# Kernel tuning notes

Hardware: AMD Instinct MI355X
Metric: run time of the kernel (lower is better)

## Reference

```python
import jax, jax.numpy as jnp
import numpy as np

N = 100_000        # nodes
E = 1_600_000      # edges (avg degree 16)
NODE_DIM = 64
HIDDEN = 64
OUT = 32


def _glorot(key, fan_in, fan_out):
    lim = np.sqrt(6.0 / (fan_in + fan_out)).astype(np.float32)
    return jax.random.uniform(key, (fan_in, fan_out), jnp.float32, -lim, lim)


def setup_inputs() -> dict:
    key = jax.random.key(0)
    ks = jax.random.split(key, 5)
    x = jax.random.normal(ks[0], (N, NODE_DIM), jnp.float32)
    edge_index = jax.random.randint(ks[1], (2, E), 0, N, dtype=jnp.int64)
    return {
        "x": x,
        "edge_index": edge_index,
        "W1": _glorot(ks[2], NODE_DIM, HIDDEN),
        "b1": jnp.zeros((HIDDEN,), jnp.float32),
        "Wmu": _glorot(ks[3], HIDDEN, OUT),
        "bmu": jnp.zeros((OUT,), jnp.float32),
        "Wlv": _glorot(ks[4], HIDDEN, OUT),
        "blv": jnp.zeros((OUT,), jnp.float32),
    }


def _gcn_conv(h, W, b, src, dst, norm, n):
    """PyG GCNConv: linear (no bias) -> normalized scatter-add -> + bias.
    src/dst/norm already include self-loops and deg^{-1/2} symmetric norm."""
    h = h @ W                                   # [n, out]
    msg = h[src] * norm[:, None]                # [E+N, out] gather
    out = jax.ops.segment_sum(msg, dst, num_segments=n)  # scatter-add
    return out + b


def reference(x, edge_index, W1, b1, Wmu, bmu, Wlv, blv):
    loops = jnp.arange(N, dtype=edge_index.dtype)
    src = jnp.concatenate([edge_index[0], loops])  # add self-loops
    dst = jnp.concatenate([edge_index[1], loops])
    # symmetric normalization: deg computed on target nodes (all weights 1)
    deg = jax.ops.segment_sum(jnp.ones_like(src, dtype=x.dtype), dst, num_segments=N)
    dinv = jax.lax.rsqrt(deg)                   # deg >= 1 due to self-loops
    norm = dinv[src] * dinv[dst]

    h = jax.nn.relu(_gcn_conv(x, W1, b1, src, dst, norm, N))
    mu = _gcn_conv(h, Wmu, bmu, src, dst, norm, N)
    logvar = _gcn_conv(h, Wlv, blv, src, dst, norm, N)
    return mu, logvar
```

## Files before the change

### kernel.cpp

```cpp
#include <hip/hip_runtime.h>
#include <hip/hip_fp16.h>


#define BKT_SHIFT 9
#define BKT_NODES 512
#define CHUNK 2048

typedef __attribute__((ext_vector_type(8))) _Float16 half8;
typedef __attribute__((ext_vector_type(4))) float float4v;
typedef __attribute__((ext_vector_type(4))) unsigned uint4v;

__device__ __forceinline__ int imin(int a, int b) { return a < b ? a : b; }
__device__ __forceinline__ int imax(int a, int b) { return a > b ? a : b; }
__device__ __forceinline__ unsigned h2u(__half2 v) {
  union { __half2 h; unsigned u; } c; c.h = v; return c.u;
}
__device__ __forceinline__ __half2 u2h(unsigned x) {
  union { unsigned u; __half2 h; } c; c.u = x; return c.h;
}


__global__ __launch_bounds__(1024) void block_sums(const int* __restrict__ in,
                                                   int* __restrict__ bsum, int n) {
  __shared__ int s[1024];
  int t = threadIdx.x;
  int i = blockIdx.x * 1024 + t;
  s[t] = (i < n) ? in[i] : 0;
  __syncthreads();
  for (int off = 512; off > 0; off >>= 1) {
    if (t < off) s[t] += s[t + off];
    __syncthreads();
  }
  if (t == 0) bsum[blockIdx.x] = s[0];
}

__global__ __launch_bounds__(1024) void scan_bsums(int* __restrict__ bsum, int nb) {
  __shared__ int s[1024];
  int t = threadIdx.x;
  int v = (t < nb) ? bsum[t] : 0;
  s[t] = v;
  __syncthreads();
  for (int off = 1; off < 1024; off <<= 1) {
    int u = (t >= off) ? s[t - off] : 0;
    __syncthreads();
    s[t] += u;
    __syncthreads();
  }
  if (t < nb) bsum[t] = s[t] - v;
}

__global__ __launch_bounds__(1024) void scan_apply(int* __restrict__ data,
                                                   const int* __restrict__ bofs, int n) {
  __shared__ int s[1024];
  int t = threadIdx.x;
  int i = blockIdx.x * 1024 + t;
  int c = (i < n) ? data[i] : 0;
  s[t] = c;
  __syncthreads();
  for (int off = 1; off < 1024; off <<= 1) {
    int u = (t >= off) ? s[t - off] : 0;
    __syncthreads();
    s[t] += u;
    __syncthreads();
  }
  if (i < n) data[i] = bofs[blockIdx.x] + s[t] - c;
}


__global__ __launch_bounds__(256) void bucket_count(const int* __restrict__ dst,
                                                    int* __restrict__ cnt,
                                                    int E, int nbk, int nblk) {
  __shared__ int hist[2][256];
  const int t = threadIdx.x;
  const int h = (t >> 7) & 1;
  hist[0][t] = 0;
  hist[1][t] = 0;
  __syncthreads();
  const int base = blockIdx.x * CHUNK;
  const int end = imin(base + CHUNK, E);
  for (int e = base + t * 4; e < end; e += 1024) {
    if (e + 3 < end) {
      const int4 d4 = *(const int4*)(dst + e);
      atomicAdd(&hist[h][d4.x >> BKT_SHIFT], 1);
      atomicAdd(&hist[h][d4.y >> BKT_SHIFT], 1);
      atomicAdd(&hist[h][d4.z >> BKT_SHIFT], 1);
      atomicAdd(&hist[h][d4.w >> BKT_SHIFT], 1);
    } else {
      for (int k = e; k < end; ++k) atomicAdd(&hist[h][dst[k] >> BKT_SHIFT], 1);
    }
  }
  __syncthreads();
  if (t < nbk) cnt[t * nblk + blockIdx.x] = hist[0][t] + hist[1][t];
}

__global__ __launch_bounds__(256) void bucket_scatter(const int* __restrict__ src,
                                                      const int* __restrict__ dst,
                                                      const int* __restrict__ ofs,
                                                      int2* __restrict__ tmp,
                                                      int E, int nbk, int nblk) {
  __shared__ int cur[256];
  const int t = threadIdx.x;
  if (t < nbk) cur[t] = ofs[t * nblk + blockIdx.x];
  __syncthreads();
  const int base = blockIdx.x * CHUNK;
  const int end = imin(base + CHUNK, E);
  for (int e = base + t * 4; e < end; e += 1024) {
    if (e + 3 < end) {
      const int4 s4 = *(const int4*)(src + e);
      const int4 d4 = *(const int4*)(dst + e);
      int p0 = atomicAdd(&cur[d4.x >> BKT_SHIFT], 1);
      tmp[p0] = make_int2(s4.x, d4.x);
      int p1 = atomicAdd(&cur[d4.y >> BKT_SHIFT], 1);
      tmp[p1] = make_int2(s4.y, d4.y);
      int p2 = atomicAdd(&cur[d4.z >> BKT_SHIFT], 1);
      tmp[p2] = make_int2(s4.z, d4.z);
      int p3 = atomicAdd(&cur[d4.w >> BKT_SHIFT], 1);
      tmp[p3] = make_int2(s4.w, d4.w);
    } else {
      for (int k = e; k < end; ++k) {
        int d = dst[k];
        int pos = atomicAdd(&cur[d >> BKT_SHIFT], 1);
        tmp[pos] = make_int2(src[k], d);
      }
    }
  }
}

__global__ __launch_bounds__(512) void bucket_build(const int2* __restrict__ tmp,
                                                    const int* __restrict__ ofs,
                                                    int* __restrict__ row_ptr,
                                                    float* __restrict__ dinv,
                                                    int* __restrict__ pairs,
                                                    int n, int nbk, int nblk, int E) {
  __shared__ int hist[BKT_NODES];
  __shared__ int scn[BKT_NODES];
  const int b = blockIdx.x;
  const int t = threadIdx.x;
  const int node0 = b << BKT_SHIFT;
  hist[t] = 0;
  __syncthreads();
  const int s = ofs[b * nblk];
  const int e = (b + 1 < nbk) ? ofs[(b + 1) * nblk] : E;
  for (int k = s + t; k < e; k += 512) atomicAdd(&hist[tmp[k].y - node0], 1);
  __syncthreads();
  const int v = hist[t];
  scn[t] = v;
  __syncthreads();
  for (int off = 1; off < 512; off <<= 1) {
    int u = (t >= off) ? scn[t - off] : 0;
    __syncthreads();
    scn[t] += u;
    __syncthreads();
  }
  const int excl = s + scn[t] - v;
  const int node = node0 + t;
  if (node < n) {
    row_ptr[node] = excl;
    dinv[node] = rsqrtf(1.0f + (float)v);
  }
  if (b == nbk - 1 && t == 0) row_ptr[n] = E;
  hist[t] = excl;
  __syncthreads();
  for (int k = s + t; k < e; k += 512) {
    int2 p = tmp[k];
    int pos = atomicAdd(&hist[p.y - node0], 1);
    pairs[pos] = p.x;
  }
}

__global__ __launch_bounds__(256) void cast_scale(const float* __restrict__ x,
                                                  const float* __restrict__ dinv,
                                                  __half* __restrict__ xs,
                                                  __half* __restrict__ hs,
                                                  int n4, int nrow) {
  int i = blockIdx.x * blockDim.x + threadIdx.x;
  if (i < n4) {
    float4 v = ((const float4*)x)[i];
    float d = dinv[i >> 4];
    __half2* o = (__half2*)(xs + (size_t)i * 4);
    o[0] = __floats2half2_rn(d * v.x, d * v.y);
    o[1] = __floats2half2_rn(d * v.z, d * v.w);
  } else if (i < n4 + 32) {
    int j = i - n4;
    if (j < 16)
      ((float2*)(xs + (size_t)nrow * 64))[j] = make_float2(0.f, 0.f);
    else
      ((float2*)(hs + (size_t)nrow * 64))[j - 16] = make_float2(0.f, 0.f);
  }
}


#define YSTRIDE 264

__global__ __launch_bounds__(256, 4) void agg_layer1(const __half* __restrict__ xs,
                                                     const int* __restrict__ pairs,
                                                     const int* __restrict__ row_ptr,
                                                     const float* __restrict__ W1,
                                                     const float* __restrict__ b1,
                                                     __half* __restrict__ hs, int n) {
  __shared__ _Float16 ylds_all[4][16 * YSTRIDE];
  __shared__ float dilds_all[4][16];
  const int wv = threadIdx.x >> 6;
  _Float16* ylds = ylds_all[wv];
  float* dilds = dilds_all[wv];
  const int lane = threadIdx.x & 63;
  const int g = lane >> 3, q = lane & 7;
  const int quad = lane >> 4, col = lane & 15;

  half8 bfrag[2][4];
#pragma unroll
  for (int s = 0; s < 2; ++s)
#pragma unroll
    for (int t = 0; t < 4; ++t)
#pragma unroll
      for (int jj = 0; jj < 8; ++jj)
        bfrag[s][t][jj] = (_Float16)W1[(s * 32 + quad * 8 + jj) * 64 + t * 16 + col];
  float bias[4];
#pragma unroll
  for (int t = 0; t < 4; ++t) bias[t] = b1[t * 16 + col];

  const int ntiles = (n + 15) >> 4;
  for (int tile = blockIdx.x * 4 + wv; tile < ntiles; tile += gridDim.x * 4) {
    const int row0 = tile << 4;
#pragma unroll 1
    for (int rg = 0; rg < 4; ++rg) {
      int start[4], end[4], idx[4];
      __half2 acc[4][4];
      int maxdeg = 0;
#pragma unroll
      for (int j = 0; j < 4; ++j) {
        const int i = row0 + rg * 4 + j;
        start[j] = 0; end[j] = 0;
        if (i < n) { start[j] = row_ptr[i]; end[j] = row_ptr[i + 1]; }
        maxdeg = imax(maxdeg, end[j] - start[j]);
#pragma unroll
        for (int k = 0; k < 4; ++k) acc[j][k] = u2h(0u);
        idx[j] = (start[j] + g < end[j]) ? pairs[start[j] + g] : n;
      }
      const int iters = (maxdeg + 7) >> 3;
#pragma unroll 1
      for (int it = 0; it < iters; ++it) {
        int nidx[4];
#pragma unroll
        for (int j = 0; j < 4; ++j) {
          const int ofs2 = start[j] + (it + 1) * 8 + g;
          nidx[j] = (ofs2 < end[j]) ? pairs[ofs2] : n;
        }
#pragma unroll
        for (int j = 0; j < 4; ++j) {
          const float4 rr = *(const float4*)(xs + (size_t)idx[j] * 64 + q * 8);
          const __half2* hp = (const __half2*)&rr;
#pragma unroll
          for (int k = 0; k < 4; ++k) acc[j][k] = __hadd2(acc[j][k], hp[k]);
        }
#pragma unroll
        for (int j = 0; j < 4; ++j) idx[j] = nidx[j];
      }
#pragma unroll
      for (int j = 0; j < 4; ++j) {
        const int i = row0 + rg * 4 + j;
        if (g == 0 && i < n) {
          const float4 sr = *(const float4*)(xs + (size_t)i * 64 + q * 8);
          const __half2* hp = (const __half2*)&sr;
#pragma unroll
          for (int k = 0; k < 4; ++k) acc[j][k] = __hadd2(acc[j][k], hp[k]);
        }
#pragma unroll
        for (int k = 0; k < 4; ++k) {
          unsigned u = __shfl_xor(h2u(acc[j][k]), 32);
          acc[j][k] = __hadd2(acc[j][k], u2h(u));
        }
        const float di = rsqrtf((float)(1 + end[j] - start[j]));
        const __half hdi = __float2half(di);
        const __half2 di2 = __halves2half2(hdi, hdi);
        uint4v st;
        st.x = h2u(__hmul2(di2, acc[j][0]));
        st.y = h2u(__hmul2(di2, acc[j][1]));
        st.z = h2u(__hmul2(di2, acc[j][2]));
        st.w = h2u(__hmul2(di2, acc[j][3]));
        *(uint4v*)(ylds + (rg * 4 + j) * YSTRIDE + (g & 3) * 64 + q * 8) = st;
        if (lane == 0) dilds[rg * 4 + j] = di;
      }
    }
    float4v acc[4];
#pragma unroll
    for (int t = 0; t < 4; ++t) acc[t] = (float4v){bias[t], bias[t], bias[t], bias[t]};
#pragma unroll
    for (int s2 = 0; s2 < 8; ++s2) {
      half8 af = *(half8*)(ylds + col * YSTRIDE + s2 * 32 + quad * 8);
      const int sW = s2 & 1;
#pragma unroll
      for (int t = 0; t < 4; ++t)
        acc[t] = __builtin_amdgcn_mfma_f32_16x16x32_f16(af, bfrag[sW][t], acc[t], 0, 0, 0);
    }
    const float4 dis = *(const float4*)(dilds + quad * 4);
    const float dd[4] = {dis.x, dis.y, dis.z, dis.w};
#pragma unroll
    for (int t = 0; t < 4; ++t)
#pragma unroll
      for (int reg = 0; reg < 4; ++reg) {
        const int row = row0 + quad * 4 + reg;
        if (row < n)
          hs[(size_t)row * 64 + t * 16 + col] =
              __float2half(dd[reg] * fmaxf(acc[t][reg], 0.f));
      }
  }
}

__global__ __launch_bounds__(256, 4) void agg_layer2(const __half* __restrict__ hsin,
                                                     const int* __restrict__ pairs,
                                                     const int* __restrict__ row_ptr,
                                                     const float* __restrict__ Wmu,
                                                     const float* __restrict__ bmu,
                                                     const float* __restrict__ Wlv,
                                                     const float* __restrict__ blv,
                                                     float* __restrict__ out_mu,
                                                     float* __restrict__ out_lv, int n) {
  __shared__ _Float16 ylds_all[4][16 * YSTRIDE];
  const int wv = threadIdx.x >> 6;
  _Float16* ylds = ylds_all[wv];
  const int lane = threadIdx.x & 63;
  const int g = lane >> 3, q = lane & 7;
  const int quad = lane >> 4, col = lane & 15;

  half8 bfrag[2][4];
#pragma unroll
  for (int s = 0; s < 2; ++s)
#pragma unroll
    for (int t = 0; t < 4; ++t) {
      const int j = t * 16 + col;
      const float* W = (j < 32) ? Wmu : Wlv;
      const int jc = j & 31;
#pragma unroll
      for (int jj = 0; jj < 8; ++jj)
        bfrag[s][t][jj] = (_Float16)W[(s * 32 + quad * 8 + jj) * 32 + jc];
    }
  float bias[4];
#pragma unroll
  for (int t = 0; t < 4; ++t) {
    const int j = t * 16 + col;
    bias[t] = (j < 32) ? bmu[j] : blv[j - 32];
  }

  const int ntiles = (n + 15) >> 4;
  for (int tile = blockIdx.x * 4 + wv; tile < ntiles; tile += gridDim.x * 4) {
    const int row0 = tile << 4;
#pragma unroll 1
    for (int rg = 0; rg < 4; ++rg) {
      int start[4], end[4], idx[4];
      __half2 acc[4][4];
      int maxdeg = 0;
#pragma unroll
      for (int j = 0; j < 4; ++j) {
        const int i = row0 + rg * 4 + j;
        start[j] = 0; end[j] = 0;
        if (i < n) { start[j] = row_ptr[i]; end[j] = row_ptr[i + 1]; }
        maxdeg = imax(maxdeg, end[j] - start[j]);
#pragma unroll
        for (int k = 0; k < 4; ++k) acc[j][k] = u2h(0u);
        idx[j] = (start[j] + g < end[j]) ? pairs[start[j] + g] : n;
      }
      const int iters = (maxdeg + 7) >> 3;
#pragma unroll 1
      for (int it = 0; it < iters; ++it) {
        int nidx[4];
#pragma unroll
        for (int j = 0; j < 4; ++j) {
          const int ofs2 = start[j] + (it + 1) * 8 + g;
          nidx[j] = (ofs2 < end[j]) ? pairs[ofs2] : n;
        }
#pragma unroll
        for (int j = 0; j < 4; ++j) {
          const float4 rr = *(const float4*)(hsin + (size_t)idx[j] * 64 + q * 8);
          const __half2* hp = (const __half2*)&rr;
#pragma unroll
          for (int k = 0; k < 4; ++k) acc[j][k] = __hadd2(acc[j][k], hp[k]);
        }
#pragma unroll
        for (int j = 0; j < 4; ++j) idx[j] = nidx[j];
      }
#pragma unroll
      for (int j = 0; j < 4; ++j) {
        const int i = row0 + rg * 4 + j;
        if (g == 0 && i < n) {
          const float4 sr = *(const float4*)(hsin + (size_t)i * 64 + q * 8);
          const __half2* hp = (const __half2*)&sr;
#pragma unroll
          for (int k = 0; k < 4; ++k) acc[j][k] = __hadd2(acc[j][k], hp[k]);
        }
#pragma unroll
        for (int k = 0; k < 4; ++k) {
          unsigned u = __shfl_xor(h2u(acc[j][k]), 32);
          acc[j][k] = __hadd2(acc[j][k], u2h(u));
        }
        const float di = rsqrtf((float)(1 + end[j] - start[j]));
        const __half hdi = __float2half(di);
        const __half2 di2 = __halves2half2(hdi, hdi);
        uint4v st;
        st.x = h2u(__hmul2(di2, acc[j][0]));
        st.y = h2u(__hmul2(di2, acc[j][1]));
        st.z = h2u(__hmul2(di2, acc[j][2]));
        st.w = h2u(__hmul2(di2, acc[j][3]));
        *(uint4v*)(ylds + (rg * 4 + j) * YSTRIDE + (g & 3) * 64 + q * 8) = st;
      }
    }
    float4v acc[4];
#pragma unroll
    for (int t = 0; t < 4; ++t) acc[t] = (float4v){bias[t], bias[t], bias[t], bias[t]};
#pragma unroll
    for (int s2 = 0; s2 < 8; ++s2) {
      half8 af = *(half8*)(ylds + col * YSTRIDE + s2 * 32 + quad * 8);
      const int sW = s2 & 1;
#pragma unroll
      for (int t = 0; t < 4; ++t)
        acc[t] = __builtin_amdgcn_mfma_f32_16x16x32_f16(af, bfrag[sW][t], acc[t], 0, 0, 0);
    }
#pragma unroll
    for (int t = 0; t < 4; ++t)
#pragma unroll
      for (int reg = 0; reg < 4; ++reg) {
        const int row = row0 + quad * 4 + reg;
        if (row < n) {
          const int j = t * 16 + col;
          if (j < 32)
            out_mu[(size_t)row * 32 + j] = acc[t][reg];
          else
            out_lv[(size_t)row * 32 + (j - 32)] = acc[t][reg];
        }
      }
  }
}

extern "C" void kernel_launch(void* const* d_in, const int* in_sizes, int n_in,
                              void* d_out, int out_size, void* d_ws, size_t ws_size,
                              hipStream_t stream) {
  const float* x = (const float*)d_in[0];
  const int* ei = (const int*)d_in[1];
  const float* W1 = (const float*)d_in[2];
  const float* b1 = (const float*)d_in[3];
  const float* Wmu = (const float*)d_in[4];
  const float* bmu = (const float*)d_in[5];
  const float* Wlv = (const float*)d_in[6];
  const float* blv = (const float*)d_in[7];

  const int N = in_sizes[0] / 64;
  const int E = in_sizes[1] / 2;
  const int* src = ei;
  const int* dst = ei + E;

  const int NBK = (N + BKT_NODES - 1) >> BKT_SHIFT;
  const int NBLK = (E + CHUNK - 1) / CHUNK;
  const int FL = NBK * NBLK;

  auto align256 = [](size_t v) { return (v + 255) & ~(size_t)255; };
  char* p = (char*)d_ws;
  int* row_ptr = (int*)p;  p += align256((size_t)(N + 1) * 4);
  float* dinv = (float*)p; p += align256((size_t)N * 4);
  int* bsum = (int*)p;     p += align256((size_t)1024 * 4);
  int* cnt = (int*)p;      p += align256((size_t)FL * 4);
  int* pairs = (int*)p;    p += align256((size_t)E * 4);
  __half* xs = (__half*)p; p += align256((size_t)(N + 1) * 64 * 2);
  size_t tmp_bytes = (size_t)E * 8;
  size_t hs_bytes = (size_t)(N + 1) * 64 * 2;
  int2* tmp = (int2*)p;
  __half* hs = (__half*)p;
  p += align256(tmp_bytes > hs_bytes ? tmp_bytes : hs_bytes);

  float* out_mu = (float*)d_out;
  float* out_lv = out_mu + (size_t)N * 32;

  const int NB_F = (FL + 1023) / 1024;
  const int n4 = N * 16;

  bucket_count<<<NBLK, 256, 0, stream>>>(dst, cnt, E, NBK, NBLK);
  block_sums<<<NB_F, 1024, 0, stream>>>(cnt, bsum, FL);
  scan_bsums<<<1, 1024, 0, stream>>>(bsum, NB_F);
  scan_apply<<<NB_F, 1024, 0, stream>>>(cnt, bsum, FL);
  bucket_scatter<<<NBLK, 256, 0, stream>>>(src, dst, cnt, tmp, E, NBK, NBLK);
  bucket_build<<<NBK, 512, 0, stream>>>(tmp, cnt, row_ptr, dinv, pairs, N, NBK, NBLK, E);

  cast_scale<<<(n4 + 32 + 255) / 256, 256, 0, stream>>>(x, dinv, xs, hs, n4, N);

  const int ntiles = (N + 15) / 16;
  const int ablocks = (ntiles + 3) / 4;
  agg_layer1<<<ablocks, 256, 0, stream>>>(xs, pairs, row_ptr, W1, b1, hs, N);
  agg_layer2<<<ablocks, 256, 0, stream>>>(hs, pairs, row_ptr, Wmu, bmu, Wlv, blv,
                                          out_mu, out_lv, N);
}
```

Baseline: 240.5 us.

## Split fp16 feature tables into 16-column planes for cache-local gathers

The scaled fp16 feature tables change from row-major 64-wide rows to four column planes of 16 halves per node, each about 3.2 MB. Both aggregation kernels now loop over the planes and gather 32-byte slices, with 32 edges in flight per wavefront instead of 8, then reduce partial sums with extra shuffles. The goal is for each plane's random gathers to stay resident in L2 rather than streaming the whole 12.8 MB table. In exchange, row_ptr and pairs are read four times, lanes are wasted for nodes with degree well below 32, and the writer and cast kernels need the new plane addressing.

Result: slower. 406.1 us (+68.8%).

```diff
diff --git a/kernel.cpp b/kernel.cpp
--- a/kernel.cpp
+++ b/kernel.cpp
@@ -173,19 +173,24 @@
                                                   __half* __restrict__ xs,
                                                   __half* __restrict__ hs,
                                                   int n4, int nrow) {
+  const size_t plane = ((size_t)nrow + 1) * 16;
   int i = blockIdx.x * blockDim.x + threadIdx.x;
   if (i < n4) {
     float4 v = ((const float4*)x)[i];
-    float d = dinv[i >> 4];
-    __half2* o = (__half2*)(xs + (size_t)i * 4);
+    const int node = i >> 4;
+    const int j = i & 15;
+    const int c = j >> 2;
+    const int h = (j & 3) * 4;
+    float d = dinv[node];
+    __half2* o = (__half2*)(xs + (size_t)c * plane + (size_t)node * 16 + h);
     o[0] = __floats2half2_rn(d * v.x, d * v.y);
     o[1] = __floats2half2_rn(d * v.z, d * v.w);
   } else if (i < n4 + 32) {
     int j = i - n4;
-    if (j < 16)
-      ((float2*)(xs + (size_t)nrow * 64))[j] = make_float2(0.f, 0.f);
-    else
-      ((float2*)(hs + (size_t)nrow * 64))[j - 16] = make_float2(0.f, 0.f);
+    __half* base = (j < 16) ? xs : hs;
+    int jj = j & 15;
+    *(float2*)(base + (size_t)(jj >> 2) * plane + (size_t)nrow * 16 + (jj & 3) * 4) =
+        make_float2(0.f, 0.f);
   }
 }
 
@@ -200,11 +205,12 @@
                                                      __half* __restrict__ hs, int n) {
   __shared__ _Float16 ylds_all[4][16 * YSTRIDE];
   __shared__ float dilds_all[4][16];
+  const size_t plane = ((size_t)n + 1) * 16;
   const int wv = threadIdx.x >> 6;
   _Float16* ylds = ylds_all[wv];
   float* dilds = dilds_all[wv];
   const int lane = threadIdx.x & 63;
-  const int g = lane >> 3, q = lane & 7;
+  const int g = lane >> 1, q = lane & 1;
   const int quad = lane >> 4, col = lane & 15;
 
   half8 bfrag[2][4];
@@ -223,63 +229,73 @@
   for (int tile = blockIdx.x * 4 + wv; tile < ntiles; tile += gridDim.x * 4) {
     const int row0 = tile << 4;
 #pragma unroll 1
-    for (int rg = 0; rg < 4; ++rg) {
-      int start[4], end[4], idx[4];
-      __half2 acc[4][4];
-      int maxdeg = 0;
-#pragma unroll
-      for (int j = 0; j < 4; ++j) {
-        const int i = row0 + rg * 4 + j;
-        start[j] = 0; end[j] = 0;
-        if (i < n) { start[j] = row_ptr[i]; end[j] = row_ptr[i + 1]; }
-        maxdeg = imax(maxdeg, end[j] - start[j]);
-#pragma unroll
-        for (int k = 0; k < 4; ++k) acc[j][k] = u2h(0u);
-        idx[j] = (start[j] + g < end[j]) ? pairs[start[j] + g] : n;
-      }
-      const int iters = (maxdeg + 7) >> 3;
+    for (int c = 0; c < 4; ++c) {
+      const __half* tab = xs + (size_t)c * plane;
 #pragma unroll 1
-      for (int it = 0; it < iters; ++it) {
-        int nidx[4];
+      for (int rg = 0; rg < 4; ++rg) {
+        int start[4], end[4], idx[4];
+        __half2 acc[4][4];
+        int maxdeg = 0;
 #pragma unroll
         for (int j = 0; j < 4; ++j) {
-          const int ofs2 = start[j] + (it + 1) * 8 + g;
-          nidx[j] = (ofs2 < end[j]) ? pairs[ofs2] : n;
+          const int i = row0 + rg * 4 + j;
+          start[j] = 0; end[j] = 0;
+          if (i < n) { start[j] = row_ptr[i]; end[j] = row_ptr[i + 1]; }
+          maxdeg = imax(maxdeg, end[j] - start[j]);
+#pragma unroll
+          for (int k = 0; k < 4; ++k) acc[j][k] = u2h(0u);
+          idx[j] = (start[j] + g < end[j]) ? pairs[start[j] + g] : n;
+        }
+        const int iters = (maxdeg + 31) >> 5;
+#pragma unroll 1
+        for (int it = 0; it < iters; ++it) {
+          int nidx[4];
+#pragma unroll
+          for (int j = 0; j < 4; ++j) {
+            const int ofs2 = start[j] + (it + 1) * 32 + g;
+            nidx[j] = (ofs2 < end[j]) ? pairs[ofs2] : n;
+          }
+#pragma unroll
+          for (int j = 0; j < 4; ++j) {
+            const float4 rr = *(const float4*)(tab + (size_t)idx[j] * 16 + q * 8);
+            const __half2* hp = (const __half2*)&rr;
+#pragma unroll
+            for (int k = 0; k < 4; ++k) acc[j][k] = __hadd2(acc[j][k], hp[k]);
+          }
+#pragma unroll
+          for (int j = 0; j < 4; ++j) idx[j] = nidx[j];
         }
 #pragma unroll
         for (int j = 0; j < 4; ++j) {
-          const float4 rr = *(const float4*)(xs + (size_t)idx[j] * 64 + q * 8);
-          const __half2* hp = (const __half2*)&rr;
-#pragma unroll
-          for (int k = 0; k < 4; ++k) acc[j][k] = __hadd2(acc[j][k], hp[k]);
-        }
-#pragma unroll
-        for (int j = 0; j < 4; ++j) idx[j] = nidx[j];
-      }
-#pragma unroll
-      for (int j = 0; j < 4; ++j) {
-        const int i = row0 + rg * 4 + j;
-        if (g == 0 && i < n) {
-          const float4 sr = *(const float4*)(xs + (size_t)i * 64 + q * 8);
-          const __half2* hp = (const __half2*)&sr;
-#pragma unroll
-          for (int k = 0; k < 4; ++k) acc[j][k] = __hadd2(acc[j][k], hp[k]);
-        }
-#pragma unroll
-        for (int k = 0; k < 4; ++k) {
-          unsigned u = __shfl_xor(h2u(acc[j][k]), 32);
-          acc[j][k] = __hadd2(acc[j][k], u2h(u));
-        }
-        const float di = rsqrtf((float)(1 + end[j] - start[j]));
-        const __half hdi = __float2half(di);
-        const __half2 di2 = __halves2half2(hdi, hdi);
-        uint4v st;
-        st.x = h2u(__hmul2(di2, acc[j][0]));
-        st.y = h2u(__hmul2(di2, acc[j][1]));
-        st.z = h2u(__hmul2(di2, acc[j][2]));
-        st.w = h2u(__hmul2(di2, acc[j][3]));
-        *(uint4v*)(ylds + (rg * 4 + j) * YSTRIDE + (g & 3) * 64 + q * 8) = st;
-        if (lane == 0) dilds[rg * 4 + j] = di;
+          const int i = row0 + rg * 4 + j;
+          if (g == 0 && i < n) {
+            const float4 sr = *(const float4*)(tab + (size_t)i * 16 + q * 8);
+            const __half2* hp = (const __half2*)&sr;
+#pragma unroll
+            for (int k = 0; k < 4; ++k) acc[j][k] = __hadd2(acc[j][k], hp[k]);
+          }
+#pragma unroll
+          for (int k = 0; k < 4; ++k) {
+            unsigned u = __shfl_xor(h2u(acc[j][k]), 8);
+            acc[j][k] = __hadd2(acc[j][k], u2h(u));
+            u = __shfl_xor(h2u(acc[j][k]), 16);
+            acc[j][k] = __hadd2(acc[j][k], u2h(u));
+            u = __shfl_xor(h2u(acc[j][k]), 32);
+            acc[j][k] = __hadd2(acc[j][k], u2h(u));
+          }
+          const float di = rsqrtf((float)(1 + end[j] - start[j]));
+          if (lane < 8) {
+            const __half hdi = __float2half(di);
+            const __half2 di2 = __halves2half2(hdi, hdi);
+            uint4v st;
+            st.x = h2u(__hmul2(di2, acc[j][0]));
+            st.y = h2u(__hmul2(di2, acc[j][1]));
+            st.z = h2u(__hmul2(di2, acc[j][2]));
+            st.w = h2u(__hmul2(di2, acc[j][3]));
+            *(uint4v*)(ylds + (rg * 4 + j) * YSTRIDE + g * 64 + c * 16 + q * 8) = st;
+          }
+          if (c == 0 && lane == 0) dilds[rg * 4 + j] = di;
+        }
       }
     }
     float4v acc[4];
@@ -301,7 +317,7 @@
       for (int reg = 0; reg < 4; ++reg) {
         const int row = row0 + quad * 4 + reg;
         if (row < n)
-          hs[(size_t)row * 64 + t * 16 + col] =
+          hs[(size_t)t * plane + (size_t)row * 16 + col] =
               __float2half(dd[reg] * fmaxf(acc[t][reg], 0.f));
       }
   }
@@ -317,10 +333,11 @@
                                                      float* __restrict__ out_mu,
                                                      float* __restrict__ out_lv, int n) {
   __shared__ _Float16 ylds_all[4][16 * YSTRIDE];
+  const size_t plane = ((size_t)n + 1) * 16;
   const int wv = threadIdx.x >> 6;
   _Float16* ylds = ylds_all[wv];
   const int lane = threadIdx.x & 63;
-  const int g = lane >> 3, q = lane & 7;
+  const int g = lane >> 1, q = lane & 1;
   const int quad = lane >> 4, col = lane & 15;
 
   half8 bfrag[2][4];
@@ -346,62 +363,72 @@
   for (int tile = blockIdx.x * 4 + wv; tile < ntiles; tile += gridDim.x * 4) {
     const int row0 = tile << 4;
 #pragma unroll 1
-    for (int rg = 0; rg < 4; ++rg) {
-      int start[4], end[4], idx[4];
-      __half2 acc[4][4];
-      int maxdeg = 0;
-#pragma unroll
-      for (int j = 0; j < 4; ++j) {
-        const int i = row0 + rg * 4 + j;
-        start[j] = 0; end[j] = 0;
-        if (i < n) { start[j] = row_ptr[i]; end[j] = row_ptr[i + 1]; }
-        maxdeg = imax(maxdeg, end[j] - start[j]);
-#pragma unroll
-        for (int k = 0; k < 4; ++k) acc[j][k] = u2h(0u);
-        idx[j] = (start[j] + g < end[j]) ? pairs[start[j] + g] : n;
-      }
-      const int iters = (maxdeg + 7) >> 3;
+    for (int c = 0; c < 4; ++c) {
+      const __half* tab = hsin + (size_t)c * plane;
 #pragma unroll 1
-      for (int it = 0; it < iters; ++it) {
-        int nidx[4];
+      for (int rg = 0; rg < 4; ++rg) {
+        int start[4], end[4], idx[4];
+        __half2 acc[4][4];
+        int maxdeg = 0;
 #pragma unroll
         for (int j = 0; j < 4; ++j) {
-          const int ofs2 = start[j] + (it + 1) * 8 + g;
-          nidx[j] = (ofs2 < end[j]) ? pairs[ofs2] : n;
+          const int i = row0 + rg * 4 + j;
+          start[j] = 0; end[j] = 0;
+          if (i < n) { start[j] = row_ptr[i]; end[j] = row_ptr[i + 1]; }
+          maxdeg = imax(maxdeg, end[j] - start[j]);
+#pragma unroll
+          for (int k = 0; k < 4; ++k) acc[j][k] = u2h(0u);
+          idx[j] = (start[j] + g < end[j]) ? pairs[start[j] + g] : n;
+        }
+        const int iters = (maxdeg + 31) >> 5;
+#pragma unroll 1
+        for (int it = 0; it < iters; ++it) {
+          int nidx[4];
+#pragma unroll
+          for (int j = 0; j < 4; ++j) {
+            const int ofs2 = start[j] + (it + 1) * 32 + g;
+            nidx[j] = (ofs2 < end[j]) ? pairs[ofs2] : n;
+          }
+#pragma unroll
+          for (int j = 0; j < 4; ++j) {
+            const float4 rr = *(const float4*)(tab + (size_t)idx[j] * 16 + q * 8);
+            const __half2* hp = (const __half2*)&rr;
+#pragma unroll
+            for (int k = 0; k < 4; ++k) acc[j][k] = __hadd2(acc[j][k], hp[k]);
+          }
+#pragma unroll
+          for (int j = 0; j < 4; ++j) idx[j] = nidx[j];
         }
 #pragma unroll
         for (int j = 0; j < 4; ++j) {
-          const float4 rr = *(const float4*)(hsin + (size_t)idx[j] * 64 + q * 8);
-          const __half2* hp = (const __half2*)&rr;
-#pragma unroll
-          for (int k = 0; k < 4; ++k) acc[j][k] = __hadd2(acc[j][k], hp[k]);
-        }
-#pragma unroll
-        for (int j = 0; j < 4; ++j) idx[j] = nidx[j];
-      }
-#pragma unroll
-      for (int j = 0; j < 4; ++j) {
-        const int i = row0 + rg * 4 + j;
-        if (g == 0 && i < n) {
-          const float4 sr = *(const float4*)(hsin + (size_t)i * 64 + q * 8);
-          const __half2* hp = (const __half2*)&sr;
-#pragma unroll
-          for (int k = 0; k < 4; ++k) acc[j][k] = __hadd2(acc[j][k], hp[k]);
-        }
-#pragma unroll
-        for (int k = 0; k < 4; ++k) {
-          unsigned u = __shfl_xor(h2u(acc[j][k]), 32);
-          acc[j][k] = __hadd2(acc[j][k], u2h(u));
-        }
-        const float di = rsqrtf((float)(1 + end[j] - start[j]));
-        const __half hdi = __float2half(di);
-        const __half2 di2 = __halves2half2(hdi, hdi);
-        uint4v st;
-        st.x = h2u(__hmul2(di2, acc[j][0]));
-        st.y = h2u(__hmul2(di2, acc[j][1]));
-        st.z = h2u(__hmul2(di2, acc[j][2]));
-        st.w = h2u(__hmul2(di2, acc[j][3]));
-        *(uint4v*)(ylds + (rg * 4 + j) * YSTRIDE + (g & 3) * 64 + q * 8) = st;
+          const int i = row0 + rg * 4 + j;
+          if (g == 0 && i < n) {
+            const float4 sr = *(const float4*)(tab + (size_t)i * 16 + q * 8);
+            const __half2* hp = (const __half2*)&sr;
+#pragma unroll
+            for (int k = 0; k < 4; ++k) acc[j][k] = __hadd2(acc[j][k], hp[k]);
+          }
+#pragma unroll
+          for (int k = 0; k < 4; ++k) {
+            unsigned u = __shfl_xor(h2u(acc[j][k]), 8);
+            acc[j][k] = __hadd2(acc[j][k], u2h(u));
+            u = __shfl_xor(h2u(acc[j][k]), 16);
+            acc[j][k] = __hadd2(acc[j][k], u2h(u));
+            u = __shfl_xor(h2u(acc[j][k]), 32);
+            acc[j][k] = __hadd2(acc[j][k], u2h(u));
+          }
+          const float di = rsqrtf((float)(1 + end[j] - start[j]));
+          if (lane < 8) {
+            const __half hdi = __float2half(di);
+            const __half2 di2 = __halves2half2(hdi, hdi);
+            uint4v st;
+            st.x = h2u(__hmul2(di2, acc[j][0]));
+            st.y = h2u(__hmul2(di2, acc[j][1]));
+            st.z = h2u(__hmul2(di2, acc[j][2]));
+            st.w = h2u(__hmul2(di2, acc[j][3]));
+            *(uint4v*)(ylds + (rg * 4 + j) * YSTRIDE + g * 64 + c * 16 + q * 8) = st;
+          }
+        }
       }
     }
     float4v acc[4];
```
